# Kernel tuning notes

Measured on AMD Instinct MI355X. Metric: run time of the kernel, lower is better.

Reference implementation:

```python
import math
import jax, jax.numpy as jnp
import numpy as np

B, L, F, H = 16, 1024, 512, 8
D = F // H
FACTOR = 5.0
KEEP_MINLEN = 15.0


def setup_inputs() -> dict:
    key = jax.random.key(0)
    ks = jax.random.split(key, 12)
    inp = {
        "query": jax.random.normal(ks[0], (B, L, F), jnp.float32),
        "key": jax.random.normal(ks[1], (B, L, F), jnp.float32),
        "value": jax.random.normal(ks[2], (B, L, F), jnp.float32),
        "mask": jnp.ones((B, 1, L), jnp.int32),
    }
    s = 0.02
    inp["Wq"] = jax.random.normal(ks[3], (F, F), jnp.float32) * s
    inp["bq"] = jnp.zeros((F,), jnp.float32)
    inp["Wk"] = jax.random.normal(ks[4], (F, F), jnp.float32) * s
    inp["bk"] = jnp.zeros((F,), jnp.float32)
    inp["Wv"] = jax.random.normal(ks[5], (F, F), jnp.float32) * s
    inp["bv"] = jnp.zeros((F,), jnp.float32)
    inp["Wo"] = jax.random.normal(ks[6], (F, F), jnp.float32) * s
    inp["bo"] = jnp.zeros((F,), jnp.float32)
    return inp


def _n_top(Lq: int) -> int:
    if Lq <= KEEP_MINLEN:
        return Lq
    u = int(round(FACTOR * math.ceil(math.log(Lq))))
    return min(u, Lq)


def reference(query, key, value, mask, Wq, bq, Wk, bk, Wv, bv, Wo, bo):
    def proj(x, W, b):
        # torch nn.Linear: x @ W.T + b ; then (B,L,H,D) -> (B,H,L,D)
        return (x @ W.T + b).reshape(B, L, H, D).transpose(0, 2, 1, 3)

    q = proj(query, Wq, bq)
    k = proj(key, Wk, bk)
    v = proj(value, Wv, bv)

    # prob_QK with index=None: full (unscaled) QK to compute sparsity measure M
    scores_full = jnp.einsum('bhqd,bhkd->bhqk', q, k)  # (B,H,L,L)
    M = scores_full.max(-1) - scores_full.mean(-1)      # (B,H,L)
    u = _n_top(L)
    _, idx = jax.lax.top_k(M, u)                        # (B,H,u)

    q_red = jnp.take_along_axis(q, idx[..., None], axis=2)  # (B,H,u,D)
    scores = jnp.einsum('bhud,bhkd->bhuk', q_red, k) / math.sqrt(D)

    neg = (mask == 0)[:, None, :, :]  # (B,1,1,L) broadcasts over heads/queries
    scores = jnp.where(neg, -jnp.inf, scores)
    attn = jax.nn.softmax(scores, axis=-1)
    attn = jnp.where(neg, 0.0, attn)

    ctx_top = jnp.einsum('bhuk,bhkd->bhud', attn, v)   # (B,H,u,D)

    # initial context = mean of V over keys, broadcast to all queries
    context = jnp.broadcast_to(v.mean(axis=2, keepdims=True), (B, H, L, D))
    bi = jnp.arange(B)[:, None, None]
    hi = jnp.arange(H)[None, :, None]
    context = context.at[bi, hi, idx].set(ctx_top)

    x = context.transpose(0, 2, 1, 3).reshape(B, L, H * D)
    return x @ Wo.T + bo
```

## Files before the change

### kernel.cpp

```cpp
#include <hip/hip_runtime.h>
#include <math.h>

#define B_ 16
#define L_ 1024
#define H_ 8
#define U_ 35

typedef float f32x4 __attribute__((ext_vector_type(4)));
typedef short bf16x8 __attribute__((ext_vector_type(8)));

__device__ __forceinline__ unsigned short f2bf(float x) {
    unsigned int u = __float_as_uint(x);
    u += 0x7FFFu + ((u >> 16) & 1u);
    return (unsigned short)(u >> 16);
}
__device__ __forceinline__ float bf2f(unsigned short b) {
    return __uint_as_float(((unsigned int)b) << 16);
}

#define MFMA(a, b, c) __builtin_amdgcn_mfma_f32_16x16x32_bf16((a), (b), (c), 0, 0, 0)

#define OFF_V      ((size_t)0)
#define OFF_QHI    ((size_t)8388608)
#define OFF_QLO    ((size_t)12582912)
#define OFF_CTXP   OFF_QHI
#define OFF_KHI    ((size_t)16777216)
#define OFF_KLO    ((size_t)20971520)
#define OFF_S      ((size_t)25165824)
#define OFF_WQH    OFF_S
#define OFF_WQL    ((size_t)(OFF_S + 131072))
#define OFF_WKH    ((size_t)(OFF_S + 262144))
#define OFF_WKL    ((size_t)(OFF_S + 393216))
#define OFF_WVH    ((size_t)(OFF_S + 524288))
#define OFF_WVL    ((size_t)(OFF_S + 655360))
#define OFF_M      ((size_t)29753344)
#define OFF_KMEAN  ((size_t)29884416)
#define OFF_VMEAN  ((size_t)29892608)
#define OFF_CTXD   ((size_t)29900800)
#define OFF_IDX    ((size_t)30187520)
#define OFF_OBASE  ((size_t)30192000)

__global__ __launch_bounds__(256) void split_w3(
    const float* __restrict__ Wq, const float* __restrict__ Wk,
    const float* __restrict__ Wv,
    unsigned short* __restrict__ wqh, unsigned short* __restrict__ wql,
    unsigned short* __restrict__ wkh, unsigned short* __restrict__ wkl,
    unsigned short* __restrict__ wvh, unsigned short* __restrict__ wvl)
{
    const int w = blockIdx.x >> 10;
    const int i = (blockIdx.x & 1023) * 256 + threadIdx.x;
    const float* W = (w == 0) ? Wq : (w == 1) ? Wk : Wv;
    unsigned short* hi = (w == 0) ? wqh : (w == 1) ? wkh : wvh;
    unsigned short* lo = (w == 0) ? wql : (w == 1) ? wkl : wvl;
    float x = W[i];
    unsigned short h = f2bf(x);
    hi[i] = h;
    lo[i] = f2bf(x - bf2f(h));
}

__global__ __launch_bounds__(256) void gemm_qkv(
    const float* __restrict__ Aq, const float* __restrict__ Ak,
    const float* __restrict__ Av,
    const unsigned short* __restrict__ wqh, const unsigned short* __restrict__ wql,
    const unsigned short* __restrict__ wkh, const unsigned short* __restrict__ wkl,
    const unsigned short* __restrict__ wvh, const unsigned short* __restrict__ wvl,
    const float* __restrict__ bqp, const float* __restrict__ bkp,
    const float* __restrict__ bvp,
    float* __restrict__ vout,
    unsigned short* __restrict__ qhi_o, unsigned short* __restrict__ qlo_o,
    unsigned short* __restrict__ khi_o, unsigned short* __restrict__ klo_o)
{
    __shared__ unsigned short Ah[128][40];
    __shared__ unsigned short Al[128][40];
    __shared__ unsigned short Bh[128][40];
    __shared__ unsigned short Bl[128][40];

    const int z = blockIdx.z;
    const float* A = (z == 0) ? Aq : (z == 1) ? Ak : Av;
    const unsigned short* Whi = (z == 0) ? wqh : (z == 1) ? wkh : wvh;
    const unsigned short* Wlo = (z == 0) ? wql : (z == 1) ? wkl : wvl;
    const float* bias = (z == 0) ? bqp : (z == 1) ? bkp : bvp;
    float* outf = (z == 2) ? vout : nullptr;
    unsigned short* ohi = (z == 0) ? qhi_o : (z == 1) ? khi_o : nullptr;
    unsigned short* olo = (z == 0) ? qlo_o : (z == 1) ? klo_o : nullptr;

    const int tid = threadIdx.x, lane = tid & 63, wave = tid >> 6;
    const int m0 = blockIdx.x * 128, n0 = blockIdx.y * 128;
    const int wm = (wave >> 1) * 64, wn = (wave & 1) * 64;

    f32x4 zero4 = {0.f, 0.f, 0.f, 0.f};
    f32x4 acc[4][4];
#pragma unroll
    for (int i = 0; i < 4; i++)
#pragma unroll
        for (int j = 0; j < 4; j++) acc[i][j] = zero4;

    const int ar = tid >> 3, ac = (tid & 7) * 4;
    const int br = tid >> 2, bc = (tid & 3) * 8;
    const int kc = (lane >> 4) * 8;
    const int fr = lane & 15;

    for (int k0 = 0; k0 < 512; k0 += 32) {
        if (k0) __syncthreads();
#pragma unroll
        for (int p = 0; p < 4; ++p) {
            float4 a4 = *(const float4*)(A + (size_t)(m0 + ar + p * 32) * 512 + k0 + ac);
            ushort4 h4, l4;
            h4.x = f2bf(a4.x); l4.x = f2bf(a4.x - bf2f(h4.x));
            h4.y = f2bf(a4.y); l4.y = f2bf(a4.y - bf2f(h4.y));
            h4.z = f2bf(a4.z); l4.z = f2bf(a4.z - bf2f(h4.z));
            h4.w = f2bf(a4.w); l4.w = f2bf(a4.w - bf2f(h4.w));
            *(ushort4*)&Ah[ar + p * 32][ac] = h4;
            *(ushort4*)&Al[ar + p * 32][ac] = l4;
        }
#pragma unroll
        for (int p = 0; p < 2; ++p) {
            size_t off = (size_t)(n0 + br + p * 64) * 512 + k0 + bc;
            *(uint4*)&Bh[br + p * 64][bc] = *(const uint4*)(Whi + off);
            *(uint4*)&Bl[br + p * 64][bc] = *(const uint4*)(Wlo + off);
        }
        __syncthreads();

        bf16x8 ah[4], al[4];
#pragma unroll
        for (int mi = 0; mi < 4; ++mi) {
            int row = wm + mi * 16 + fr;
            ah[mi] = *(bf16x8*)&Ah[row][kc];
            al[mi] = *(bf16x8*)&Al[row][kc];
        }
#pragma unroll
        for (int ni = 0; ni < 4; ++ni) {
            int rn = wn + ni * 16 + fr;
            bf16x8 bh8 = *(bf16x8*)&Bh[rn][kc];
            bf16x8 bl8 = *(bf16x8*)&Bl[rn][kc];
#pragma unroll
            for (int mi = 0; mi < 4; ++mi) {
                acc[mi][ni] = MFMA(ah[mi], bh8, acc[mi][ni]);
                acc[mi][ni] = MFMA(ah[mi], bl8, acc[mi][ni]);
                acc[mi][ni] = MFMA(al[mi], bh8, acc[mi][ni]);
            }
        }
    }

    const int col = lane & 15, rq = (lane >> 4) * 4;
#pragma unroll
    for (int ni = 0; ni < 4; ++ni) {
        int n = n0 + wn + ni * 16 + col;
        float bn = bias[n];
#pragma unroll
        for (int mi = 0; mi < 4; ++mi) {
#pragma unroll
            for (int r = 0; r < 4; ++r) {
                int m = m0 + wm + mi * 16 + rq + r;
                float val = acc[mi][ni][r] + bn;
                size_t off = ((size_t)((m >> 10) * H_ + (n >> 6)) * L_ + (m & 1023)) * 64 + (n & 63);
                if (outf) outf[off] = val;
                if (ohi) {
                    unsigned short h = f2bf(val);
                    ohi[off] = h;
                    olo[off] = f2bf(val - bf2f(h));
                }
            }
        }
    }
}

__global__ __launch_bounds__(256) void means_fused(
    const unsigned short* __restrict__ khi, const unsigned short* __restrict__ klo,
    const float* __restrict__ v, float* __restrict__ kmean, float* __restrict__ vmean)
{
    const int which = blockIdx.x >> 7;
    const int bh = blockIdx.x & 127;
    const int d = threadIdx.x & 63, g = threadIdx.x >> 6;
    __shared__ float red[4][64];
    float s = 0.f;
    if (which == 0) {
        size_t base = ((size_t)bh * L_ + g * 256) * 64 + d;
#pragma unroll 8
        for (int l = 0; l < 256; l++) {
            size_t o = base + (size_t)l * 64;
            s += bf2f(khi[o]) + bf2f(klo[o]);
        }
    } else {
        const float* p = v + ((size_t)bh * L_ + g * 256) * 64 + d;
#pragma unroll 8
        for (int l = 0; l < 256; l++) s += p[(size_t)l * 64];
    }
    red[g][d] = s;
    __syncthreads();
    if (threadIdx.x < 64) {
        const int dd = threadIdx.x;
        float m = (red[0][dd] + red[1][dd] + red[2][dd] + red[3][dd]) * (1.0f / 1024.0f);
        (which == 0 ? kmean : vmean)[(size_t)bh * 64 + dd] = m;
    }
}

__global__ __launch_bounds__(256) void qk_rowmax_mfma(
    const unsigned short* __restrict__ qhi, const unsigned short* __restrict__ qlo,
    const unsigned short* __restrict__ khi, const unsigned short* __restrict__ klo,
    const float* __restrict__ kmean, float* __restrict__ Mout)
{
    __shared__ unsigned short Qh[64][72], Ql[64][72];
    __shared__ unsigned short Kh[64][72], Kl[64][72];
    __shared__ float Mred[64][4];
    __shared__ float km[64];
    const int bh = blockIdx.x, q0 = blockIdx.y * 64;
    const int tid = threadIdx.x, lane = tid & 63, wave = tid >> 6;

    if (tid < 64) km[tid] = kmean[bh * 64 + tid];
    {
        int r = tid >> 2, c = (tid & 3) * 16;
        size_t off = ((size_t)bh * L_ + q0 + r) * 64 + c;
        *(uint4*)&Qh[r][c]     = *(const uint4*)(qhi + off);
        *(uint4*)&Qh[r][c + 8] = *(const uint4*)(qhi + off + 8);
        *(uint4*)&Ql[r][c]     = *(const uint4*)(qlo + off);
        *(uint4*)&Ql[r][c + 8] = *(const uint4*)(qlo + off + 8);
    }

    const size_t kb = (size_t)bh * L_ * 64;
    const int sr = tid >> 2, sc = (tid & 3) * 16;
    const int fr = lane & 15;
    f32x4 zero4 = {0.f, 0.f, 0.f, 0.f};

    uint4 pha, phb, pla, plb;
    {
        size_t off = kb + (size_t)sr * 64 + sc;
        pha = *(const uint4*)(khi + off);  phb = *(const uint4*)(khi + off + 8);
        pla = *(const uint4*)(klo + off);  plb = *(const uint4*)(klo + off + 8);
    }

    __syncthreads();

    bf16x8 qah[2][4], qal[2][4];
#pragma unroll
    for (int ks = 0; ks < 2; ++ks) {
        int kcol = ks * 32 + (lane >> 4) * 8;
#pragma unroll
        for (int mi = 0; mi < 4; ++mi) {
            qah[ks][mi] = *(bf16x8*)&Qh[mi * 16 + fr][kcol];
            qal[ks][mi] = *(bf16x8*)&Ql[mi * 16 + fr][kcol];
        }
    }

    float rmax[4][4];
#pragma unroll
    for (int mi = 0; mi < 4; ++mi)
#pragma unroll
        for (int r = 0; r < 4; ++r) rmax[mi][r] = -INFINITY;

    for (int kt = 0; kt < 16; ++kt) {
        if (kt) __syncthreads();
        *(uint4*)&Kh[sr][sc] = pha;  *(uint4*)&Kh[sr][sc + 8] = phb;
        *(uint4*)&Kl[sr][sc] = pla;  *(uint4*)&Kl[sr][sc + 8] = plb;
        __syncthreads();

        if (kt < 15) {
            size_t off = kb + (size_t)((kt + 1) * 64 + sr) * 64 + sc;
            pha = *(const uint4*)(khi + off);  phb = *(const uint4*)(khi + off + 8);
            pla = *(const uint4*)(klo + off);  plb = *(const uint4*)(klo + off + 8);
        }

        f32x4 acc[4];
#pragma unroll
        for (int mi = 0; mi < 4; ++mi) acc[mi] = zero4;

#pragma unroll
        for (int ks = 0; ks < 2; ++ks) {
            int kcol = ks * 32 + (lane >> 4) * 8;
            int krow = wave * 16 + fr;
            bf16x8 bh8 = *(bf16x8*)&Kh[krow][kcol];
            bf16x8 bl8 = *(bf16x8*)&Kl[krow][kcol];
#pragma unroll
            for (int mi = 0; mi < 4; ++mi) {
                acc[mi] = MFMA(qah[ks][mi], bh8, acc[mi]);
                acc[mi] = MFMA(qah[ks][mi], bl8, acc[mi]);
                acc[mi] = MFMA(qal[ks][mi], bh8, acc[mi]);
            }
        }
#pragma unroll
        for (int mi = 0; mi < 4; ++mi)
#pragma unroll
            for (int r = 0; r < 4; ++r)
                rmax[mi][r] = fmaxf(rmax[mi][r], acc[mi][r]);
    }

#pragma unroll
    for (int mi = 0; mi < 4; ++mi)
#pragma unroll
        for (int r = 0; r < 4; ++r) {
            float v = rmax[mi][r];
            v = fmaxf(v, __shfl_xor(v, 1));
            v = fmaxf(v, __shfl_xor(v, 2));
            v = fmaxf(v, __shfl_xor(v, 4));
            v = fmaxf(v, __shfl_xor(v, 8));
            rmax[mi][r] = v;
        }
    if ((lane & 15) == 0) {
        int quad = lane >> 4;
#pragma unroll
        for (int mi = 0; mi < 4; ++mi)
#pragma unroll
            for (int r = 0; r < 4; ++r)
                Mred[mi * 16 + quad * 4 + r][wave] = rmax[mi][r];
    }
    __syncthreads();
    if (tid < 64) {
        float mx = fmaxf(fmaxf(Mred[tid][0], Mred[tid][1]),
                         fmaxf(Mred[tid][2], Mred[tid][3]));
        float dot = 0.f;
#pragma unroll 4
        for (int d = 0; d < 64; ++d)
            dot = fmaf(bf2f(Qh[tid][d]) + bf2f(Ql[tid][d]), km[d], dot);
        Mout[(size_t)bh * L_ + q0 + tid] = mx - dot;
    }
}

__global__ __launch_bounds__(256) void topk35(
    const float* __restrict__ Min, int* __restrict__ idx_out)
{
    const int bh = blockIdx.x;
    const int tid = threadIdx.x;
    __shared__ float vals[1024];
    __shared__ float wv[4];
    __shared__ int wi[4];
    for (int i = tid; i < 1024; i += 256) vals[i] = Min[(size_t)bh * 1024 + i];
    __syncthreads();
    for (int it = 0; it < U_; ++it) {
        float bv = -INFINITY; int bi = 1 << 30;
        for (int i = tid; i < 1024; i += 256) {
            float x = vals[i];
            if (x > bv) { bv = x; bi = i; }
        }
#pragma unroll
        for (int off = 32; off; off >>= 1) {
            float ov = __shfl_down(bv, off);
            int   oi = __shfl_down(bi, off);
            if (ov > bv || (ov == bv && oi < bi)) { bv = ov; bi = oi; }
        }
        if ((tid & 63) == 0) { wv[tid >> 6] = bv; wi[tid >> 6] = bi; }
        __syncthreads();
        if (tid == 0) {
#pragma unroll
            for (int w = 1; w < 4; ++w) {
                if (wv[w] > bv || (wv[w] == bv && wi[w] < bi)) { bv = wv[w]; bi = wi[w]; }
            }
            idx_out[bh * U_ + it] = bi;
            vals[bi] = -INFINITY;
        }
        __syncthreads();
    }
}

__global__ __launch_bounds__(256) void scores_red(
    const unsigned short* __restrict__ qhi, const unsigned short* __restrict__ qlo,
    const unsigned short* __restrict__ khi, const unsigned short* __restrict__ klo,
    const int* __restrict__ idx, const int* __restrict__ mask,
    float* __restrict__ S)
{
    __shared__ float Qs[64][36];
    __shared__ float Ks[64][68];
    const int bh = blockIdx.x;
    const int b = bh >> 3;
    const int tid = threadIdx.x;
    const int tk = tid & 63, tg = tid >> 6;

    for (int t = tid; t < 36 * 64; t += 256) {
        int u = t >> 6, d = t & 63;
        float val = 0.f;
        if (u < U_) {
            int l = idx[bh * U_ + u];
            size_t off = ((size_t)bh * L_ + l) * 64 + d;
            val = bf2f(qhi[off]) + bf2f(qlo[off]);
        }
        Qs[d][u] = val;
    }

    const size_t kb = (size_t)bh * L_ * 64;
    const int sr = tid >> 2, sc = (tid & 3) * 16;
    float acc[9];
    const int kt0 = blockIdx.y * 2;
    for (int ki = 0; ki < 2; ++ki) {
        int kt = kt0 + ki;
        if (ki) __syncthreads();
        {
            size_t off = kb + (size_t)(kt * 64 + sr) * 64 + sc;
            uint4 h0 = *(const uint4*)(khi + off);
            uint4 h1 = *(const uint4*)(khi + off + 8);
            uint4 l0 = *(const uint4*)(klo + off);
            uint4 l1 = *(const uint4*)(klo + off + 8);
            unsigned short hv[16], lv[16];
            *(uint4*)hv = h0; *(uint4*)(hv + 8) = h1;
            *(uint4*)lv = l0; *(uint4*)(lv + 8) = l1;
#pragma unroll
            for (int i = 0; i < 16; ++i)
                Ks[sc + i][sr] = bf2f(hv[i]) + bf2f(lv[i]);
        }
        __syncthreads();
#pragma unroll
        for (int j = 0; j < 9; j++) acc[j] = 0.f;
#pragma unroll 4
        for (int d = 0; d < 64; ++d) {
            float kv = Ks[d][tk];
#pragma unroll
            for (int j = 0; j < 9; j++) acc[j] = fmaf(Qs[d][tg + 4 * j], kv, acc[j]);
        }
        const int kcol = kt * 64 + tk;
        const bool msk = (mask[b * L_ + kcol] == 0);
#pragma unroll
        for (int j = 0; j < 9; j++) {
            int u = tg + 4 * j;
            if (u < U_)
                S[((size_t)bh * U_ + u) * 1024 + kcol] = msk ? -INFINITY : acc[j] * 0.125f;
        }
    }
}

__global__ __launch_bounds__(256) void softmax_rows(float* __restrict__ S)
{
    const size_t base = (size_t)blockIdx.x * 1024;
    const int tid = threadIdx.x;
    __shared__ float redm[4];
    __shared__ float reds[4];
    float4 v = *(const float4*)(S + base + tid * 4);
    float mx = fmaxf(fmaxf(v.x, v.y), fmaxf(v.z, v.w));
#pragma unroll
    for (int off = 32; off; off >>= 1) mx = fmaxf(mx, __shfl_down(mx, off));
    if ((tid & 63) == 0) redm[tid >> 6] = mx;
    __syncthreads();
    mx = fmaxf(fmaxf(redm[0], redm[1]), fmaxf(redm[2], redm[3]));
    float e0 = __expf(v.x - mx), e1 = __expf(v.y - mx);
    float e2 = __expf(v.z - mx), e3 = __expf(v.w - mx);
    float s = e0 + e1 + e2 + e3;
#pragma unroll
    for (int off = 32; off; off >>= 1) s += __shfl_down(s, off);
    if ((tid & 63) == 0) reds[tid >> 6] = s;
    __syncthreads();
    s = reds[0] + reds[1] + reds[2] + reds[3];
    const float inv = 1.0f / s;
    float4 o; o.x = e0 * inv; o.y = e1 * inv; o.z = e2 * inv; o.w = e3 * inv;
    *(float4*)(S + base + tid * 4) = o;
}

__global__ __launch_bounds__(256) void ctx_partial(
    const float* __restrict__ S, const float* __restrict__ v,
    float* __restrict__ ctxp)
{
    __shared__ float Vs[128][68];
    __shared__ float Wt[36][128];
    const int bh = blockIdx.x, kc = blockIdx.y;
    const int tid = threadIdx.x;
    const int td = tid & 63, tg = tid >> 6;
    const int lr = tid >> 2, lc0 = (tid & 3) * 16;

    const float* vbase = v + ((size_t)bh * L_ + kc * 128) * 64;
    const float* Sbase = S + (size_t)bh * U_ * 1024 + kc * 128;

#pragma unroll
    for (int hh = 0; hh < 2; ++hh) {
        int row = lr + hh * 64;
        const float* src = vbase + (size_t)row * 64 + lc0;
        *(float4*)&Vs[row][lc0 + 0]  = *(const float4*)(src + 0);
        *(float4*)&Vs[row][lc0 + 4]  = *(const float4*)(src + 4);
        *(float4*)&Vs[row][lc0 + 8]  = *(const float4*)(src + 8);
        *(float4*)&Vs[row][lc0 + 12] = *(const float4*)(src + 12);
    }
    for (int t = tid; t < 36 * 128; t += 256) {
        int u = t >> 7, kk = t & 127;
        Wt[u][kk] = (u < U_) ? Sbase[(size_t)u * 1024 + kk] : 0.f;
    }
    __syncthreads();

    float acc[9];
#pragma unroll
    for (int j = 0; j < 9; j++) acc[j] = 0.f;
#pragma unroll 2
    for (int kk = 0; kk < 128; ++kk) {
        float vv = Vs[kk][td];
#pragma unroll
        for (int j = 0; j < 9; j++) acc[j] = fmaf(Wt[tg + 4 * j][kk], vv, acc[j]);
    }
#pragma unroll
    for (int j = 0; j < 9; j++) {
        int u = tg + 4 * j;
        if (u < U_)
            ctxp[((size_t)(kc * 128 + bh) * 36 + u) * 64 + td] = acc[j];
    }
}

__global__ __launch_bounds__(256) void ctx_reduce_diff(
    const float* __restrict__ ctxp, const float* __restrict__ vmean,
    float* __restrict__ ctxd)
{
    const int i = blockIdx.x * 256 + threadIdx.x;
    const int d = i & 63;
    const int rest = i >> 6;
    const int u = rest % U_;
    const int bh = rest / U_;
    float s = 0.f;
#pragma unroll
    for (int kc = 0; kc < 8; ++kc)
        s += ctxp[((size_t)(kc * 128 + bh) * 36 + u) * 64 + d];
    ctxd[i] = s - vmean[(size_t)bh * 64 + d];
}

__global__ __launch_bounds__(256) void vmean_proj(
    const float* __restrict__ vmean, const float* __restrict__ Wo,
    const float* __restrict__ bo, float* __restrict__ obase)
{
    const int b = blockIdx.x >> 3, n0 = (blockIdx.x & 7) * 64;
    const int tid = threadIdx.x;
    __shared__ float xbar[512];
    __shared__ float psum[64][5];
    for (int i = tid; i < 512; i += 256)
        xbar[i] = vmean[(size_t)(b * 8 + (i >> 6)) * 64 + (i & 63)];
    __syncthreads();
    const int n = n0 + (tid >> 2), fq = (tid & 3) * 128;
    float s = 0.f;
    for (int f = 0; f < 128; f += 4) {
        float4 w = *(const float4*)(Wo + (size_t)n * 512 + fq + f);
        s += xbar[fq + f] * w.x + xbar[fq + f + 1] * w.y +
             xbar[fq + f + 2] * w.z + xbar[fq + f + 3] * w.w;
    }
    psum[tid >> 2][tid & 3] = s;
    __syncthreads();
    if (tid < 64)
        obase[(size_t)b * 512 + n0 + tid] =
            psum[tid][0] + psum[tid][1] + psum[tid][2] + psum[tid][3] + bo[n0 + tid];
}

__global__ void broadcast_out(const float* __restrict__ obase, float* __restrict__ out)
{
    const size_t e = ((size_t)blockIdx.x * 256 + threadIdx.x) * 4;
    const int n = (int)(e & 511);
    const int b = (int)(e >> 19);
    *(float4*)(out + e) = *(const float4*)(obase + (b << 9) + n);
}

__global__ __launch_bounds__(128) void delta_out(
    const float* __restrict__ ctxd, const int* __restrict__ idx,
    const float* __restrict__ Wo, float* __restrict__ out)
{
    const int bh = blockIdx.x, b = bh >> 3, h = bh & 7;
    const int tid = threadIdx.x;
    const int n = blockIdx.y * 128 + tid;
    __shared__ float sd[U_][64];
    __shared__ int ls[U_];
    if (tid < U_) ls[tid] = idx[bh * U_ + tid];
    for (int t = tid; t < U_ * 64; t += 128)
        sd[t >> 6][t & 63] = ctxd[(size_t)bh * U_ * 64 + t];

    float4 w[16];
    const float* wp = Wo + (size_t)n * 512 + h * 64;
#pragma unroll
    for (int jc = 0; jc < 16; ++jc) w[jc] = *(const float4*)(wp + jc * 4);
    __syncthreads();

    for (int u = 0; u < U_; ++u) {
        float acc = 0.f;
#pragma unroll
        for (int jc = 0; jc < 16; ++jc) {
            float4 dv = *(const float4*)&sd[u][jc * 4];
            acc = fmaf(dv.w, w[jc].w, fmaf(dv.z, w[jc].z,
                  fmaf(dv.y, w[jc].y, fmaf(dv.x, w[jc].x, acc))));
        }
        atomicAdd(out + ((size_t)b * L_ + ls[u]) * 512 + n, acc);
    }
}

extern "C" void kernel_launch(void* const* d_in, const int* in_sizes, int n_in,
                              void* d_out, int out_size, void* d_ws, size_t ws_size,
                              hipStream_t stream)
{
    (void)in_sizes; (void)n_in; (void)out_size; (void)ws_size;
    const float* query = (const float*)d_in[0];
    const float* key   = (const float*)d_in[1];
    const float* value = (const float*)d_in[2];
    const int*   mask  = (const int*)d_in[3];
    const float* Wq = (const float*)d_in[4];
    const float* bq = (const float*)d_in[5];
    const float* Wk = (const float*)d_in[6];
    const float* bk = (const float*)d_in[7];
    const float* Wv = (const float*)d_in[8];
    const float* bvp = (const float*)d_in[9];
    const float* Wo = (const float*)d_in[10];
    const float* bo = (const float*)d_in[11];
    float* out = (float*)d_out;

    float* ws = (float*)d_ws;
    float* v      = ws + OFF_V;
    unsigned short* q_hi = (unsigned short*)(ws + OFF_QHI);
    unsigned short* q_lo = (unsigned short*)(ws + OFF_QLO);
    unsigned short* k_hi = (unsigned short*)(ws + OFF_KHI);
    unsigned short* k_lo = (unsigned short*)(ws + OFF_KLO);
    float* ctxp   = ws + OFF_CTXP;
    float* S      = ws + OFF_S;
    float* Marr   = ws + OFF_M;
    float* kmean  = ws + OFF_KMEAN;
    float* vmean  = ws + OFF_VMEAN;
    float* ctxd   = ws + OFF_CTXD;
    int*   idx    = (int*)(ws + OFF_IDX);
    float* obase  = ws + OFF_OBASE;
    unsigned short* wqh = (unsigned short*)(ws + OFF_WQH);
    unsigned short* wql = (unsigned short*)(ws + OFF_WQL);
    unsigned short* wkh = (unsigned short*)(ws + OFF_WKH);
    unsigned short* wkl = (unsigned short*)(ws + OFF_WKL);
    unsigned short* wvh = (unsigned short*)(ws + OFF_WVH);
    unsigned short* wvl = (unsigned short*)(ws + OFF_WVL);

    split_w3<<<3072, 256, 0, stream>>>(Wq, Wk, Wv, wqh, wql, wkh, wkl, wvh, wvl);

    gemm_qkv<<<dim3(128, 4, 3), 256, 0, stream>>>(
        query, key, value,
        wqh, wql, wkh, wkl, wvh, wvl,
        bq, bk, bvp,
        v, q_hi, q_lo, k_hi, k_lo);

    means_fused<<<256, 256, 0, stream>>>(k_hi, k_lo, v, kmean, vmean);
    vmean_proj<<<128, 256, 0, stream>>>(vmean, Wo, bo, obase);

    qk_rowmax_mfma<<<dim3(128, 16), 256, 0, stream>>>(q_hi, q_lo, k_hi, k_lo, kmean, Marr);
    topk35<<<128, 256, 0, stream>>>(Marr, idx);

    scores_red<<<dim3(128, 8), 256, 0, stream>>>(q_hi, q_lo, k_hi, k_lo, idx, mask, S);
    softmax_rows<<<B_ * H_ * U_, 256, 0, stream>>>(S);
    ctx_partial<<<dim3(128, 8), 256, 0, stream>>>(S, v, ctxp);
    ctx_reduce_diff<<<1120, 256, 0, stream>>>(ctxp, vmean, ctxd);

    broadcast_out<<<8192, 256, 0, stream>>>(obase, out);
    delta_out<<<dim3(128, 4), 128, 0, stream>>>(ctxd, idx, Wo, out);
}
```

Measured before the change: 461.3 us.

## Stage QKV GEMM epilogue through LDS and load weights via global_load_lds

The QKV projection kernel now loads the bf16 weight tiles straight into LDS with global_load_lds, which skips the register round trip. Its epilogue writes the accumulators to a shared float tile, one 64-column head half at a time, and then stores coalesced 16-byte vectors for V (fp32) and for the Q/K hi/lo bf16 planes, replacing scattered 2- and 4-byte stores. This targets uncoalesced output writes and load overhead, at the cost of extra barriers and LDS reuse. The B tile drops its padding, which may cause LDS bank conflicts on the MFMA operand reads.

```diff
diff --git a/kernel.cpp b/kernel.cpp
--- a/kernel.cpp
+++ b/kernel.cpp
@@ -16,6 +16,12 @@
 }
 __device__ __forceinline__ float bf2f(unsigned short b) {
     return __uint_as_float(((unsigned int)b) << 16);
+}
+
+__device__ __forceinline__ void gl_lds16(const void* g, void* l) {
+    __builtin_amdgcn_global_load_lds(
+        (const __attribute__((address_space(1))) unsigned int*)g,
+        (__attribute__((address_space(3))) unsigned int*)l, 16, 0, 0);
 }
 
 #define MFMA(a, b, c) __builtin_amdgcn_mfma_f32_16x16x32_bf16((a), (b), (c), 0, 0, 0)
@@ -70,17 +76,18 @@
     unsigned short* __restrict__ qhi_o, unsigned short* __restrict__ qlo_o,
     unsigned short* __restrict__ khi_o, unsigned short* __restrict__ klo_o)
 {
-    __shared__ unsigned short Ah[128][40];
-    __shared__ unsigned short Al[128][40];
-    __shared__ unsigned short Bh[128][40];
-    __shared__ unsigned short Bl[128][40];
+    __shared__ __align__(16) unsigned char smem[36864];
+    unsigned short (*Ah)[40] = (unsigned short (*)[40])(smem);
+    unsigned short (*Al)[40] = (unsigned short (*)[40])(smem + 10240);
+    unsigned short (*Bh)[32] = (unsigned short (*)[32])(smem + 20480);
+    unsigned short (*Bl)[32] = (unsigned short (*)[32])(smem + 28672);
+    float (*Cf)[68] = (float (*)[68])(smem);
 
     const int z = blockIdx.z;
     const float* A = (z == 0) ? Aq : (z == 1) ? Ak : Av;
     const unsigned short* Whi = (z == 0) ? wqh : (z == 1) ? wkh : wvh;
     const unsigned short* Wlo = (z == 0) ? wql : (z == 1) ? wkl : wvl;
     const float* bias = (z == 0) ? bqp : (z == 1) ? bkp : bvp;
-    float* outf = (z == 2) ? vout : nullptr;
     unsigned short* ohi = (z == 0) ? qhi_o : (z == 1) ? khi_o : nullptr;
     unsigned short* olo = (z == 0) ? qlo_o : (z == 1) ? klo_o : nullptr;
 
@@ -96,12 +103,20 @@
         for (int j = 0; j < 4; j++) acc[i][j] = zero4;
 
     const int ar = tid >> 3, ac = (tid & 7) * 4;
-    const int br = tid >> 2, bc = (tid & 3) * 8;
     const int kc = (lane >> 4) * 8;
     const int fr = lane & 15;
+    const int btr = tid >> 2;
+    const int btc = (tid & 3) * 8;
+    const int bldsoff = tid * 16;
 
     for (int k0 = 0; k0 < 512; k0 += 32) {
         if (k0) __syncthreads();
+#pragma unroll
+        for (int i = 0; i < 2; ++i) {
+            size_t gb = (size_t)(n0 + i * 64 + btr) * 512 + k0 + btc;
+            gl_lds16(Whi + gb, (unsigned char*)Bh + i * 4096 + bldsoff);
+            gl_lds16(Wlo + gb, (unsigned char*)Bl + i * 4096 + bldsoff);
+        }
 #pragma unroll
         for (int p = 0; p < 4; ++p) {
             float4 a4 = *(const float4*)(A + (size_t)(m0 + ar + p * 32) * 512 + k0 + ac);
@@ -113,12 +128,6 @@
             *(ushort4*)&Ah[ar + p * 32][ac] = h4;
             *(ushort4*)&Al[ar + p * 32][ac] = l4;
         }
-#pragma unroll
-        for (int p = 0; p < 2; ++p) {
-            size_t off = (size_t)(n0 + br + p * 64) * 512 + k0 + bc;
-            *(uint4*)&Bh[br + p * 64][bc] = *(const uint4*)(Whi + off);
-            *(uint4*)&Bl[br + p * 64][bc] = *(const uint4*)(Wlo + off);
-        }
         __syncthreads();
 
         bf16x8 ah[4], al[4];
@@ -143,23 +152,47 @@
     }
 
     const int col = lane & 15, rq = (lane >> 4) * 4;
-#pragma unroll
-    for (int ni = 0; ni < 4; ++ni) {
-        int n = n0 + wn + ni * 16 + col;
-        float bn = bias[n];
-#pragma unroll
-        for (int mi = 0; mi < 4; ++mi) {
-#pragma unroll
-            for (int r = 0; r < 4; ++r) {
-                int m = m0 + wm + mi * 16 + rq + r;
-                float val = acc[mi][ni][r] + bn;
-                size_t off = ((size_t)((m >> 10) * H_ + (n >> 6)) * L_ + (m & 1023)) * 64 + (n & 63);
-                if (outf) outf[off] = val;
-                if (ohi) {
-                    unsigned short h = f2bf(val);
-                    ohi[off] = h;
-                    olo[off] = f2bf(val - bf2f(h));
+    const int b_ = m0 >> 10;
+    const int l0 = m0 & 1023;
+
+#pragma unroll
+    for (int half = 0; half < 2; ++half) {
+        __syncthreads();
+        if ((wave & 1) == half) {
+#pragma unroll
+            for (int ni = 0; ni < 4; ++ni) {
+                float bn = bias[n0 + half * 64 + ni * 16 + col];
+#pragma unroll
+                for (int mi = 0; mi < 4; ++mi)
+#pragma unroll
+                    for (int r = 0; r < 4; ++r)
+                        Cf[wm + mi * 16 + rq + r][ni * 16 + col] = acc[mi][ni][r] + bn;
+            }
+        }
+        __syncthreads();
+        const int h_ = (n0 >> 6) + half;
+        const size_t plane = ((size_t)(b_ * H_ + h_) * L_ + l0) * 64;
+        if (z == 2) {
+            const int r = tid >> 1, d0 = (tid & 1) * 32;
+#pragma unroll
+            for (int j = 0; j < 8; ++j) {
+                float4 val = *(const float4*)&Cf[r][d0 + j * 4];
+                *(float4*)(vout + plane + (size_t)r * 64 + d0 + j * 4) = val;
+            }
+        } else {
+            const int r = tid >> 1, d0 = (tid & 1) * 32;
+#pragma unroll
+            for (int c = 0; c < 4; ++c) {
+                union { unsigned short s[8]; uint4 u; } ph, pl;
+#pragma unroll
+                for (int j = 0; j < 8; ++j) {
+                    float x = Cf[r][d0 + c * 8 + j];
+                    unsigned short h = f2bf(x);
+                    ph.s[j] = h;
+                    pl.s[j] = f2bf(x - bf2f(h));
                 }
+                *(uint4*)(ohi + plane + (size_t)r * 64 + d0 + c * 8) = ph.u;
+                *(uint4*)(olo + plane + (size_t)r * 64 + d0 + c * 8) = pl.u;
             }
         }
     }
```

Result: no change. 452.6 us (-1.9%).
